# Performance work log

Hardware: AMD Instinct MI355X
Metric: run time of the kernel (lower is better)

## Reference

```python
import math
import jax, jax.numpy as jnp
import numpy as np

K = 7  # kernel_size
PAD = 3  # padding (kernel_size//2)


def _base_kernels():
    # 4 oriented anisotropic Gaussian kernels, [4, K, K]
    sigma1, sigma2 = 2.5, 1.0
    ax = jnp.linspace(-(K // 2), K // 2, K)
    xx, yy = jnp.meshgrid(ax, ax, indexing='ij')
    ks = []
    for theta in (0.0, math.pi / 4, math.pi / 2, 3 * math.pi / 4):
        c, s = math.cos(theta), math.sin(theta)
        x_rot = xx * c + yy * s
        y_rot = -xx * s + yy * c
        k = jnp.exp(-(x_rot ** 2 / (2 * sigma1 ** 2) + y_rot ** 2 / (2 * sigma2 ** 2)))
        ks.append(k / k.sum())
    return jnp.stack(ks, axis=0)


def setup_inputs() -> dict:
    key = jax.random.key(0)
    ks = jax.random.split(key, 8)
    B, C, H, W, mid = 2, 256, 256, 256, 16
    x = jax.random.normal(ks[0], (B, C, H, W), dtype=jnp.float32)
    angle_map = jax.random.uniform(ks[1], (B, H, W), dtype=jnp.float32) * math.pi
    reduce_w = jax.random.normal(ks[2], (mid, C), dtype=jnp.float32) * (1.0 / math.sqrt(C))
    expand_w = jax.random.normal(ks[3], (C, mid), dtype=jnp.float32) * (1.0 / math.sqrt(mid))
    w1 = jax.random.normal(ks[4], (8, 2), dtype=jnp.float32) * (1.0 / math.sqrt(2))
    b1 = jnp.zeros((8,), dtype=jnp.float32)
    w2 = jax.random.normal(ks[5], (4, 8), dtype=jnp.float32) * (1.0 / math.sqrt(8))
    b2 = jnp.zeros((4,), dtype=jnp.float32)
    return {"x": x, "angle_map": angle_map, "reduce_w": reduce_w,
            "expand_w": expand_w, "w1": w1, "b1": b1, "w2": w2, "b2": b2}


def reference(x, angle_map, reduce_w, expand_w, w1, b1, w2, b2):
    B, C, H, W = x.shape
    mid = reduce_w.shape[0]
    base = _base_kernels()  # [4,K,K], constant buffer

    # 1x1 reduce conv
    x_low = jnp.einsum('bchw,mc->bmhw', x, reduce_w)  # [B,mid,H,W]

    # per-pixel mixing weights from angle: MLP(2->8->4) + softmax
    angle_feat = jnp.stack([jnp.sin(2 * angle_map), jnp.cos(2 * angle_map)], axis=-1)  # [B,H,W,2]
    h = jax.nn.relu(jnp.einsum('bhwi,oi->bhwo', angle_feat, w1) + b1)
    weights = jax.nn.softmax(jnp.einsum('bhwi,oi->bhwo', h, w2) + b2, axis=-1)  # [B,H,W,4]

    # reflect pad, then cross-correlate each channel with the 4 base kernels.
    # Equivalent to the original unfold+einsum: out = sum_k w_k * (x_low * base_k)
    x_pad = jnp.pad(x_low, ((0, 0), (0, 0), (PAD, PAD), (PAD, PAD)), mode='reflect')
    Hp, Wp = x_pad.shape[-2:]
    y = jax.lax.conv_general_dilated(
        x_pad.reshape(B * mid, 1, Hp, Wp), base[:, None],  # [4,1,K,K]
        window_strides=(1, 1), padding='VALID')  # [B*mid,4,H,W]
    y = y.reshape(B, mid, 4, H, W)

    out_low = jnp.einsum('bmkhw,bhwk->bmhw', y, weights)  # [B,mid,H,W]
    out = jnp.einsum('bmhw,cm->bchw', out_low, expand_w)  # 1x1 expand conv
    return out
```

## Files before the change

### kernel.cpp

```cpp
#include <hip/hip_runtime.h>

#define H_   256
#define W_   256
#define HW_  65536
#define C_   256
#define MID  16
#define B_   2

__global__ __launch_bounds__(256) void k0_prep(float* __restrict__ base_out) {
    __shared__ float s_k[4][49];
    __shared__ float s_inv[4];
    int t = threadIdx.x;
    if (t < 196) {
        int k = t / 49, p = t % 49;
        int i = p / 7, j = p % 7;
        float xx = (float)(i - 3), yy = (float)(j - 3);
        const float cs[4] = {1.0f, 0.70710678118654752f, 0.0f, -0.70710678118654752f};
        const float sn[4] = {0.0f, 0.70710678118654752f, 1.0f, 0.70710678118654752f};
        float c = cs[k], s = sn[k];
        float xr = xx * c + yy * s;
        float yr = -xx * s + yy * c;
        float v = expf(-(xr * xr * 0.08f + yr * yr * 0.5f));
        s_k[k][p] = v;
    }
    __syncthreads();
    if (t < 4) {
        float s = 0.f;
        for (int p = 0; p < 49; ++p) s += s_k[t][p];
        s_inv[t] = 1.0f / s;
    }
    __syncthreads();
    if (t < 196) base_out[t] = s_k[t / 49][t % 49] * s_inv[t / 49];
}

__global__ __launch_bounds__(256) void kA_reduce(const float* __restrict__ x,
                                                 const float* __restrict__ rw,
                                                 float* __restrict__ xlow) {
    int bh = blockIdx.x;
    int b = bh >> 8, h = bh & 255;
    int w = threadIdx.x;
    const float* xp = x + (size_t)b * C_ * HW_ + h * W_ + w;
    float acc[MID];
#pragma unroll
    for (int m = 0; m < MID; ++m) acc[m] = 0.f;
    for (int cb = 0; cb < C_; cb += 32) {
        float xv[32];
#pragma unroll
        for (int i = 0; i < 32; ++i)
            xv[i] = __builtin_nontemporal_load(xp + (size_t)(cb + i) * HW_);
#pragma unroll
        for (int i = 0; i < 32; ++i) {
#pragma unroll
            for (int m = 0; m < MID; ++m)
                acc[m] = fmaf(rw[m * C_ + cb + i], xv[i], acc[m]);
        }
    }
    float* op = xlow + (size_t)b * MID * HW_ + h * W_ + w;
#pragma unroll
    for (int m = 0; m < MID; ++m) op[(size_t)m * HW_] = acc[m];
}

__global__ __launch_bounds__(256) void kBC_conv_expand(
        const float* __restrict__ xlow,
        const float* __restrict__ base,
        const float* __restrict__ angle,
        const float* __restrict__ w1,
        const float* __restrict__ b1,
        const float* __restrict__ w2,
        const float* __restrict__ b2,
        const float* __restrict__ ew,
        float* __restrict__ out) {
    int bh = blockIdx.x;
    int b = bh >> 8, h = bh & 255;
    int w = threadIdx.x;

    float a2 = 2.0f * angle[(size_t)b * HW_ + h * W_ + w];
    float f0 = __sinf(a2), f1 = __cosf(a2);
    float hb[8];
#pragma unroll
    for (int j = 0; j < 8; ++j)
        hb[j] = fmaxf(fmaf(w1[j * 2], f0, fmaf(w1[j * 2 + 1], f1, b1[j])), 0.f);
    float lg[4];
#pragma unroll
    for (int k = 0; k < 4; ++k) {
        float s = b2[k];
#pragma unroll
        for (int j = 0; j < 8; ++j) s = fmaf(w2[k * 8 + j], hb[j], s);
        lg[k] = s;
    }
    float mx = fmaxf(fmaxf(lg[0], lg[1]), fmaxf(lg[2], lg[3]));
    float wk[4];
    float ssum = 0.f;
#pragma unroll
    for (int k = 0; k < 4; ++k) { wk[k] = __expf(lg[k] - mx); ssum += wk[k]; }
    float inv = 1.0f / ssum;
#pragma unroll
    for (int k = 0; k < 4; ++k) wk[k] *= inv;

    int cc[7];
#pragma unroll
    for (int dx = 0; dx < 7; ++dx) {
        int c0 = w + dx - 3;
        cc[dx] = c0 < 0 ? -c0 : (c0 > 255 ? 510 - c0 : c0);
    }
    float acc[MID];
#pragma unroll
    for (int m = 0; m < MID; ++m) acc[m] = 0.f;
    const float* xb = xlow + (size_t)b * MID * HW_;
    for (int dy = 0; dy < 7; ++dy) {
        int hy = h + dy - 3;
        hy = hy < 0 ? -hy : (hy > 255 ? 510 - hy : hy);
        float e[7];
#pragma unroll
        for (int dx = 0; dx < 7; ++dx) {
            int tp = dy * 7 + dx;
            e[dx] = fmaf(wk[0], base[tp],
                    fmaf(wk[1], base[49 + tp],
                    fmaf(wk[2], base[98 + tp], wk[3] * base[147 + tp])));
        }
        const float* rowb = xb + (size_t)hy * W_;
#pragma unroll
        for (int m = 0; m < MID; ++m) {
            const float* row = rowb + (size_t)m * HW_;
            float s = acc[m];
#pragma unroll
            for (int dx = 0; dx < 7; ++dx) s = fmaf(e[dx], row[cc[dx]], s);
            acc[m] = s;
        }
    }

    float* ob = out + (size_t)b * C_ * HW_ + h * W_ + w;
#pragma unroll 4
    for (int c = 0; c < C_; ++c) {
        const float* wc = ew + (size_t)c * MID;
        float s = wc[0] * acc[0];
#pragma unroll
        for (int m = 1; m < MID; ++m) s = fmaf(wc[m], acc[m], s);
        __builtin_nontemporal_store(s, ob + (size_t)c * HW_);
    }
}

extern "C" void kernel_launch(void* const* d_in, const int* in_sizes, int n_in,
                              void* d_out, int out_size, void* d_ws, size_t ws_size,
                              hipStream_t stream) {
    const float* x     = (const float*)d_in[0];
    const float* angle = (const float*)d_in[1];
    const float* rw    = (const float*)d_in[2];
    const float* ew    = (const float*)d_in[3];
    const float* w1    = (const float*)d_in[4];
    const float* b1    = (const float*)d_in[5];
    const float* w2    = (const float*)d_in[6];
    const float* b2    = (const float*)d_in[7];
    float* out = (float*)d_out;

    float* wsf  = (float*)d_ws;
    float* base = wsf;
    float* xlow = wsf + 256;

    hipLaunchKernelGGL(k0_prep,   dim3(1),   dim3(256), 0, stream, base);
    hipLaunchKernelGGL(kA_reduce, dim3(512), dim3(256), 0, stream, x, rw, xlow);
    hipLaunchKernelGGL(kBC_conv_expand, dim3(512), dim3(256), 0, stream,
                       xlow, base, angle, w1, b1, w2, b2, ew, out);
}
```

Before: 356.4 us.

## Split reduce over channel quarters and separate conv from expand kernel

The 1x1 reduce now splits its 256 input channels into four quarters, each handled by its own block that processes two pixels per thread with 64-bit loads. Partial sums go to a workspace and a new summation kernel combines them. The fused conv+expand kernel is split into a conv kernel, which writes pixel-major 16-channel intermediates, and an expand kernel spread over four channel-quarter blocks per row. The aim is more blocks in flight on the bandwidth-bound reduce and expand stages, at the cost of extra intermediate traffic and two more launches.

```diff
diff --git a/kernel.cpp b/kernel.cpp
--- a/kernel.cpp
+++ b/kernel.cpp
@@ -35,41 +35,66 @@
 
 __global__ __launch_bounds__(256) void kA_reduce(const float* __restrict__ x,
                                                  const float* __restrict__ rw,
-                                                 float* __restrict__ xlow) {
-    int bh = blockIdx.x;
-    int b = bh >> 8, h = bh & 255;
-    int w = threadIdx.x;
-    const float* xp = x + (size_t)b * C_ * HW_ + h * W_ + w;
-    float acc[MID];
-#pragma unroll
-    for (int m = 0; m < MID; ++m) acc[m] = 0.f;
-    for (int cb = 0; cb < C_; cb += 32) {
-        float xv[32];
-#pragma unroll
-        for (int i = 0; i < 32; ++i)
-            xv[i] = __builtin_nontemporal_load(xp + (size_t)(cb + i) * HW_);
-#pragma unroll
-        for (int i = 0; i < 32; ++i) {
-#pragma unroll
-            for (int m = 0; m < MID; ++m)
-                acc[m] = fmaf(rw[m * C_ + cb + i], xv[i], acc[m]);
+                                                 float* __restrict__ part) {
+    int bid = blockIdx.x;
+    int cq = bid & 3;
+    int rest = bid >> 2;
+    int b = rest >> 7, hh = rest & 127;
+    int t = threadIdx.x;
+    int pix = hh * 512 + 2 * t;
+    const unsigned long long* xp =
+        (const unsigned long long*)(x + (size_t)b * C_ * HW_ + (size_t)cq * 64 * HW_ + pix);
+    const float* wp = rw + cq * 64;
+    float accx[MID], accy[MID];
+#pragma unroll
+    for (int m = 0; m < MID; ++m) { accx[m] = 0.f; accy[m] = 0.f; }
+    for (int cb = 0; cb < 64; cb += 16) {
+        unsigned long long xv[16];
+#pragma unroll
+        for (int i = 0; i < 16; ++i)
+            xv[i] = __builtin_nontemporal_load(xp + (size_t)(cb + i) * (HW_ / 2));
+#pragma unroll
+        for (int i = 0; i < 16; ++i) {
+            float vx = __uint_as_float((unsigned)(xv[i] & 0xffffffffull));
+            float vy = __uint_as_float((unsigned)(xv[i] >> 32));
+#pragma unroll
+            for (int m = 0; m < MID; ++m) {
+                float wv = wp[m * C_ + cb + i];
+                accx[m] = fmaf(wv, vx, accx[m]);
+                accy[m] = fmaf(wv, vy, accy[m]);
+            }
         }
     }
-    float* op = xlow + (size_t)b * MID * HW_ + h * W_ + w;
-#pragma unroll
-    for (int m = 0; m < MID; ++m) op[(size_t)m * HW_] = acc[m];
-}
-
-__global__ __launch_bounds__(256) void kBC_conv_expand(
-        const float* __restrict__ xlow,
-        const float* __restrict__ base,
-        const float* __restrict__ angle,
-        const float* __restrict__ w1,
-        const float* __restrict__ b1,
-        const float* __restrict__ w2,
-        const float* __restrict__ b2,
-        const float* __restrict__ ew,
-        float* __restrict__ out) {
+    float2* op = (float2*)(part + (((size_t)cq * B_ + b) * MID) * HW_ + pix);
+#pragma unroll
+    for (int m = 0; m < MID; ++m) op[m * (HW_ / 2)] = make_float2(accx[m], accy[m]);
+}
+
+__global__ __launch_bounds__(256) void kS_sum(const float* __restrict__ part,
+                                              float* __restrict__ xlow) {
+    size_t i = (size_t)blockIdx.x * 256 + threadIdx.x;
+    const size_t stride = (size_t)B_ * MID * HW_ / 4;
+    const float4* p = (const float4*)part;
+    float4 a = p[i];
+    float4 b = p[i + stride];
+    float4 c = p[i + 2 * stride];
+    float4 d = p[i + 3 * stride];
+    float4 r;
+    r.x = (a.x + b.x) + (c.x + d.x);
+    r.y = (a.y + b.y) + (c.y + d.y);
+    r.z = (a.z + b.z) + (c.z + d.z);
+    r.w = (a.w + b.w) + (c.w + d.w);
+    ((float4*)xlow)[i] = r;
+}
+
+__global__ __launch_bounds__(256) void kB_conv(const float* __restrict__ xlow,
+                                               const float* __restrict__ base,
+                                               const float* __restrict__ angle,
+                                               const float* __restrict__ w1,
+                                               const float* __restrict__ b1,
+                                               const float* __restrict__ w2,
+                                               const float* __restrict__ b2,
+                                               float* __restrict__ olow) {
     int bh = blockIdx.x;
     int b = bh >> 8, h = bh & 255;
     int w = threadIdx.x;
@@ -129,14 +154,46 @@
         }
     }
 
-    float* ob = out + (size_t)b * C_ * HW_ + h * W_ + w;
-#pragma unroll 4
-    for (int c = 0; c < C_; ++c) {
-        const float* wc = ew + (size_t)c * MID;
-        float s = wc[0] * acc[0];
-#pragma unroll
-        for (int m = 1; m < MID; ++m) s = fmaf(wc[m], acc[m], s);
-        __builtin_nontemporal_store(s, ob + (size_t)c * HW_);
+    float4* op = (float4*)(olow + ((size_t)b * HW_ + h * W_ + w) * MID);
+    op[0] = make_float4(acc[0], acc[1], acc[2], acc[3]);
+    op[1] = make_float4(acc[4], acc[5], acc[6], acc[7]);
+    op[2] = make_float4(acc[8], acc[9], acc[10], acc[11]);
+    op[3] = make_float4(acc[12], acc[13], acc[14], acc[15]);
+}
+
+__global__ __launch_bounds__(256) void kC_expand(const float* __restrict__ olow,
+                                                 const float* __restrict__ ew,
+                                                 float* __restrict__ out) {
+    int bid = blockIdx.x;
+    int cq = bid & 3;
+    int h = (bid >> 2) & 255;
+    int b = bid >> 10;
+    int w = threadIdx.x;
+    const float4* ip = (const float4*)(olow + ((size_t)b * HW_ + h * W_ + w) * MID);
+    float4 m0 = ip[0], m1 = ip[1], m2 = ip[2], m3 = ip[3];
+    float* ob = out + ((size_t)b * C_ + cq * 64) * HW_ + h * W_ + w;
+    const float* wb = ew + (size_t)cq * 64 * MID;
+#pragma unroll 8
+    for (int ci = 0; ci < 64; ++ci) {
+        const float* wc = wb + ci * MID;
+        float s;
+        s = wc[0] * m0.x;
+        s = fmaf(wc[1], m0.y, s);
+        s = fmaf(wc[2], m0.z, s);
+        s = fmaf(wc[3], m0.w, s);
+        s = fmaf(wc[4], m1.x, s);
+        s = fmaf(wc[5], m1.y, s);
+        s = fmaf(wc[6], m1.z, s);
+        s = fmaf(wc[7], m1.w, s);
+        s = fmaf(wc[8], m2.x, s);
+        s = fmaf(wc[9], m2.y, s);
+        s = fmaf(wc[10], m2.z, s);
+        s = fmaf(wc[11], m2.w, s);
+        s = fmaf(wc[12], m3.x, s);
+        s = fmaf(wc[13], m3.y, s);
+        s = fmaf(wc[14], m3.z, s);
+        s = fmaf(wc[15], m3.w, s);
+        __builtin_nontemporal_store(s, ob + (size_t)ci * HW_);
     }
 }
 
@@ -156,9 +213,13 @@
     float* wsf  = (float*)d_ws;
     float* base = wsf;
     float* xlow = wsf + 256;
-
-    hipLaunchKernelGGL(k0_prep,   dim3(1),   dim3(256), 0, stream, base);
-    hipLaunchKernelGGL(kA_reduce, dim3(512), dim3(256), 0, stream, x, rw, xlow);
-    hipLaunchKernelGGL(kBC_conv_expand, dim3(512), dim3(256), 0, stream,
-                       xlow, base, angle, w1, b1, w2, b2, ew, out);
-}
+    float* olow = xlow + (size_t)B_ * MID * HW_;
+    float* part = olow + (size_t)B_ * MID * HW_;
+
+    hipLaunchKernelGGL(k0_prep,   dim3(1),    dim3(256), 0, stream, base);
+    hipLaunchKernelGGL(kA_reduce, dim3(1024), dim3(256), 0, stream, x, rw, part);
+    hipLaunchKernelGGL(kS_sum,    dim3(2048), dim3(256), 0, stream, part, xlow);
+    hipLaunchKernelGGL(kB_conv,   dim3(512),  dim3(256), 0, stream,
+                       xlow, base, angle, w1, b1, w2, b2, olow);
+    hipLaunchKernelGGL(kC_expand, dim3(2048), dim3(256), 0, stream, olow, ew, out);
+}
```

Measured after the change: 285.8 us. -19.8%, faster.
